# Kernel tuning notes

Measured on AMD Instinct MI355X. Metric: run time of the kernel, lower is better.

Reference implementation:

```python
import jax, jax.numpy as jnp
import numpy as np

BETA = 0.5  # exp-sum normalization exponent (not a true softmax)


def setup_inputs() -> dict:
    key = jax.random.key(0)
    ks = jax.random.split(key, 12)
    b, h = 1024, 200
    item_num, region_num, user_num = 50000, 1000, 10000
    d, hid = 128, 128  # embed_size == hidden_size (required by the bmm reshape)
    std = 0.01
    return {
        "history": jax.random.randint(ks[0], (1, b, h), 0, item_num),
        "target": jax.random.randint(ks[1], (1, b), 0, item_num),
        "history_region": jax.random.randint(ks[2], (1, b, h), 0, region_num),
        "target_region": jax.random.randint(ks[3], (1, b), 0, region_num),
        "history_visit_rate": jax.random.uniform(ks[4], (1, h), dtype=jnp.float32),
        "dist_mat": jax.random.uniform(ks[5], (b, h), dtype=jnp.float32),
        "uid": 7,
        "embed_target": std * jax.random.normal(ks[6], (item_num, d // 2), dtype=jnp.float32),
        "embed_region": std * jax.random.normal(ks[7], (region_num, d // 2), dtype=jnp.float32),
        "embed_dist": std * jax.random.normal(ks[8], (user_num, region_num), dtype=jnp.float32),
        "Wq": jax.random.normal(ks[9], (hid, d), dtype=jnp.float32) * (1.0 / np.sqrt(d)),
        "Wk": jax.random.normal(ks[10], (hid, d), dtype=jnp.float32) * (1.0 / np.sqrt(d)),
        "Wv": jax.random.normal(ks[11], (d, d), dtype=jnp.float32) * (1.0 / np.sqrt(d)),
    }


def reference(history, target, history_region, target_region, history_visit_rate,
              dist_mat, uid, embed_target, embed_region, embed_dist, Wq, Wk, Wv):
    h_idx = history[0]            # [b, h]
    tgt = target[0]               # [b]
    hr = history_region[0]        # [b, h]
    tr = target_region[0]         # [b]
    hv = history_visit_rate[0]    # [h]
    b, hlen = h_idx.shape

    # embedding gathers + concat (target half | region half)
    hist_emb = jnp.concatenate([embed_target[h_idx], embed_region[hr]], axis=-1)  # [b,h,d]
    tgt_emb = jnp.concatenate([embed_target[tgt], embed_region[tr]], axis=-1)     # [b,d]
    hd = embed_dist[uid][hr]      # [b, h]
    td = embed_dist[uid][tr]      # [b]
    d = tgt_emb.shape[1]

    # QKV projections (torch Linear: y = x @ W.T)
    q = tgt_emb @ Wq.T            # [b, d]  (hidden == d)
    k = hist_emb @ Wk.T           # [b, h, d]
    v = hist_emb @ Wv.T           # [b, h, d]

    # faithful to original: key reshaped (NOT transposed) to [b, d, h]
    k_r = k.reshape(b, d, hlen)
    scores = jnp.einsum('bd,bdh->bh', q, k_r) / jnp.sqrt(jnp.float32(d))  # [b,h]

    # exp / beta-normalized attention with equality mask
    mask = (h_idx != tgt[:, None]).astype(scores.dtype)
    exp_A = jnp.exp(scores) * mask                          # [b,h]
    exp_sum = jnp.sum(exp_A, axis=-1) ** BETA               # [b]
    attn = exp_A / exp_sum[:, None]                         # [b,h]

    # geo weights: td @ hd is a vector-matrix product -> [h], broadcast over b
    geo = jnp.exp(-1.0 / (jax.nn.relu(td @ hd) + 1.0) * dist_mat)  # [b,h]

    result1 = v * (attn + geo)[..., None]                   # [b,h,d]
    result2 = hist_emb * jnp.broadcast_to(hv, (b, hlen))[..., None]
    result = result1 + result2                              # [b,h,d]

    pred = jnp.einsum('bhd,bd->b', result, tgt_emb)         # bmm + sum over h
    return jax.nn.sigmoid(pred)
```

## Files before the change

### kernel.cpp

```cpp
#include <hip/hip_runtime.h>

typedef unsigned short USH;
typedef unsigned int   UIN;

static constexpr int Bn = 1024;
static constexpr int Hn = 200;
static constexpr int Dn = 128;
static constexpr int Dh = 64;
static constexpr int NITEM = 50000;
static constexpr int NREG  = 1000;
static constexpr int MT = 64;
static constexpr int AB_A_BLOCKS = (NITEM + MT - 1) / MT;
static constexpr int AB_B_BLOCKS = (NREG  + MT - 1) / MT;
static constexpr int WTS = 132;
static constexpr int ETS = 69;

__device__ __forceinline__ float bf2f(USH u) {
  return __uint_as_float(((UIN)u) << 16);
}
__device__ __forceinline__ float2 pb2f2(UIN p) {
  float2 r;
  r.x = __uint_as_float(p << 16);
  r.y = __uint_as_float(p & 0xffff0000u);
  return r;
}
__device__ __forceinline__ USH f2b(float f) {
  UIN x = __float_as_uint(f);
  return (USH)((x + 0x7fffu + ((x >> 16) & 1u)) >> 16);
}

__global__ __launch_bounds__(256) void g_kernel(
    const int* __restrict__ hregion, const int* __restrict__ tregion,
    const float* __restrict__ embed_dist, const int* __restrict__ uid,
    float* __restrict__ g) {
  int c = threadIdx.x;
  const float* row = embed_dist + (size_t)uid[0] * NREG;
  float acc = 0.f;
  int ibase = blockIdx.x * 16;
  for (int ii = 0; ii < 16; ii++) {
    int i = ibase + ii;
    float td = row[tregion[i]];
    if (c < Hn) acc += td * row[hregion[(size_t)i * Hn + c]];
  }
  if (c < Hn) atomicAdd(&g[c], acc);
}

__global__ __launch_bounds__(256, 2) void ab_kernel(
    const float* __restrict__ Et, const float* __restrict__ Er,
    const float* __restrict__ Wk, USH* __restrict__ A, USH* __restrict__ Bt) {
  __shared__ float wt[64 * WTS];
  __shared__ float et[MT * ETS];
  int blk = blockIdx.x, tid = threadIdx.x;
  const float* E; USH* Out; int nmax, base, koff;
  if (blk < AB_A_BLOCKS) { E = Et; Out = A;  nmax = NITEM; base = blk * MT; koff = 0; }
  else { E = Er; Out = Bt; nmax = NREG; base = (blk - AB_A_BLOCKS) * MT; koff = 64; }

#pragma unroll
  for (int p = 0; p < 8; p++) {
    int idx = p * 256 + tid;
    int row = idx >> 4, c4 = idx & 15;
    float4 w = *reinterpret_cast<const float4*>(Wk + (size_t)row * Dn + koff + c4 * 4);
    wt[(c4 * 4 + 0) * WTS + row] = w.x;
    wt[(c4 * 4 + 1) * WTS + row] = w.y;
    wt[(c4 * 4 + 2) * WTS + row] = w.z;
    wt[(c4 * 4 + 3) * WTS + row] = w.w;
  }
#pragma unroll
  for (int p = 0; p < 4; p++) {
    int idx = p * 256 + tid;
    int m = idx >> 4, c4 = idx & 15;
    int gi = base + m;
    float4 e = make_float4(0.f, 0.f, 0.f, 0.f);
    if (gi < nmax) e = *reinterpret_cast<const float4*>(E + (size_t)gi * Dh + c4 * 4);
    et[m * ETS + c4 * 4 + 0] = e.x;
    et[m * ETS + c4 * 4 + 1] = e.y;
    et[m * ETS + c4 * 4 + 2] = e.z;
    et[m * ETS + c4 * 4 + 3] = e.w;
  }
  __syncthreads();

  int jt = tid & 15, it = tid >> 4;
  const float* wb = wt + jt * 8;
  const float* eb = et + (it * 4) * ETS;
  float c[4][8];
#pragma unroll
  for (int ii = 0; ii < 4; ii++)
#pragma unroll
    for (int jj = 0; jj < 8; jj++) c[ii][jj] = 0.f;

#pragma unroll 2
  for (int k = 0; k < 64; k++) {
    float4 w0 = *reinterpret_cast<const float4*>(wb + (size_t)k * WTS);
    float4 w1 = *reinterpret_cast<const float4*>(wb + (size_t)k * WTS + 4);
    float e0 = eb[k], e1 = eb[ETS + k], e2 = eb[2 * ETS + k], e3 = eb[3 * ETS + k];
    c[0][0] += e0 * w0.x; c[0][1] += e0 * w0.y; c[0][2] += e0 * w0.z; c[0][3] += e0 * w0.w;
    c[0][4] += e0 * w1.x; c[0][5] += e0 * w1.y; c[0][6] += e0 * w1.z; c[0][7] += e0 * w1.w;
    c[1][0] += e1 * w0.x; c[1][1] += e1 * w0.y; c[1][2] += e1 * w0.z; c[1][3] += e1 * w0.w;
    c[1][4] += e1 * w1.x; c[1][5] += e1 * w1.y; c[1][6] += e1 * w1.z; c[1][7] += e1 * w1.w;
    c[2][0] += e2 * w0.x; c[2][1] += e2 * w0.y; c[2][2] += e2 * w0.z; c[2][3] += e2 * w0.w;
    c[2][4] += e2 * w1.x; c[2][5] += e2 * w1.y; c[2][6] += e2 * w1.z; c[2][7] += e2 * w1.w;
    c[3][0] += e3 * w0.x; c[3][1] += e3 * w0.y; c[3][2] += e3 * w0.z; c[3][3] += e3 * w0.w;
    c[3][4] += e3 * w1.x; c[3][5] += e3 * w1.y; c[3][6] += e3 * w1.z; c[3][7] += e3 * w1.w;
  }

#pragma unroll
  for (int ii = 0; ii < 4; ii++) {
    int item = base + it * 4 + ii;
    if (item < nmax) {
      uint4 pk;
      pk.x = (UIN)f2b(c[ii][0]) | ((UIN)f2b(c[ii][1]) << 16);
      pk.y = (UIN)f2b(c[ii][2]) | ((UIN)f2b(c[ii][3]) << 16);
      pk.z = (UIN)f2b(c[ii][4]) | ((UIN)f2b(c[ii][5]) << 16);
      pk.w = (UIN)f2b(c[ii][6]) | ((UIN)f2b(c[ii][7]) << 16);
      *reinterpret_cast<uint4*>(Out + (size_t)item * Dn + jt * 8) = pk;
    }
  }
}

__global__ __launch_bounds__(256, 2) void main_kernel(
    const int* __restrict__ history, const int* __restrict__ target,
    const int* __restrict__ hregion, const int* __restrict__ tregion,
    const float* __restrict__ hv, const float* __restrict__ dist_mat,
    const float* __restrict__ Et, const float* __restrict__ Er,
    const float* __restrict__ Wq, const float* __restrict__ Wv,
    const float* __restrict__ g, const USH* __restrict__ A,
    const USH* __restrict__ Bt, float* __restrict__ out) {
  __shared__ USH kvs[Hn * Dn];
  __shared__ float tgtE[128], qv[128], uv[128];
  __shared__ float qp[256], up[256];
  __shared__ int li[Hn], lr[Hn];
  __shared__ float red[8];
  int i = blockIdx.x, tid = threadIdx.x, lane = tid & 63, wave = tid >> 6;
  int tgt_i = target[i], tr_i = tregion[i];
  const int* hrow = history + (size_t)i * Hn;
  const int* rrow = hregion + (size_t)i * Hn;

  if (tid < Hn) { li[tid] = hrow[tid]; lr[tid] = rrow[tid]; }
  if (tid < 64)       tgtE[tid] = Et[(size_t)tgt_i * Dh + tid];
  else if (tid < 128) tgtE[tid] = Er[(size_t)tr_i * Dh + (tid - 64)];
  __syncthreads();

  {
    int rlane = tid & 31, rgrp = tid >> 5;
#pragma unroll 5
    for (int p = 0; p < 25; p++) {
      int t = p * 8 + rgrp;
      int ia = li[t], ib = lr[t];
      uint2 av = *reinterpret_cast<const uint2*>(A  + (size_t)ia * Dn + rlane * 4);
      uint2 bv = *reinterpret_cast<const uint2*>(Bt + (size_t)ib * Dn + rlane * 4);
      float2 a0 = pb2f2(av.x), a1 = pb2f2(av.y);
      float2 b0 = pb2f2(bv.x), b1 = pb2f2(bv.y);
      uint2 pk;
      pk.x = (UIN)f2b(a0.x + b0.x) | ((UIN)f2b(a0.y + b0.y) << 16);
      pk.y = (UIN)f2b(a1.x + b1.x) | ((UIN)f2b(a1.y + b1.y) << 16);
      *reinterpret_cast<uint2*>(&kvs[t * Dn + rlane * 4]) = pk;
    }
  }

  {
    int jq = tid & 127, hq = tid >> 7;
    const float4* wqp = reinterpret_cast<const float4*>(Wq + (size_t)jq * Dn + hq * 64);
    float qa = 0.f;
#pragma unroll
    for (int k4 = 0; k4 < 16; k4++) {
      float4 w = wqp[k4];
      const float* tv = &tgtE[hq * 64 + k4 * 4];
      qa += w.x * tv[0] + w.y * tv[1] + w.z * tv[2] + w.w * tv[3];
    }
    qp[tid] = qa;
    float ua = 0.f;
#pragma unroll 8
    for (int jj = 0; jj < 64; jj++)
      ua += Wv[(size_t)(hq * 64 + jj) * Dn + jq] * tgtE[hq * 64 + jj];
    up[tid] = ua;
  }
  __syncthreads();
  if (tid < 128) {
    qv[tid] = (qp[tid] + qp[tid + 128]) * 0.088388347648318447f;
    uv[tid] = up[tid] + up[tid + 128];
  }
  __syncthreads();

  float ea = 0.f, sc1 = 0.f, sc2 = 0.f;
  if (tid < Hn) {
    int c = tid;
    float acc = 0.f;
    const USH* kp = &kvs[c];
#pragma unroll 16
    for (int a = 0; a < 128; a++) acc += qv[a] * bf2f(kp[a * 200]);
    int t = tid;
    const float4* ep = reinterpret_cast<const float4*>(Et + (size_t)li[t] * Dh);
    const float4* rp = reinterpret_cast<const float4*>(Er + (size_t)lr[t] * Dh);
    float p1 = 0.f, p2 = 0.f;
#pragma unroll
    for (int k4 = 0; k4 < 16; k4++) {
      float4 e = ep[k4], r = rp[k4];
      const float* u0 = &uv[k4 * 4];        const float* t0 = &tgtE[k4 * 4];
      const float* u1 = &uv[64 + k4 * 4];   const float* t1 = &tgtE[64 + k4 * 4];
      p1 += e.x * u0[0] + e.y * u0[1] + e.z * u0[2] + e.w * u0[3]
          + r.x * u1[0] + r.y * u1[1] + r.z * u1[2] + r.w * u1[3];
      p2 += e.x * t0[0] + e.y * t0[1] + e.z * t0[2] + e.w * t0[3]
          + r.x * t1[0] + r.y * t1[1] + r.z * t1[2] + r.w * t1[3];
    }
    sc1 = p1; sc2 = p2;
    ea = (li[tid] != tgt_i) ? __expf(acc) : 0.f;
  }

  float wsum = ea;
  for (int off = 32; off > 0; off >>= 1) wsum += __shfl_down(wsum, off, 64);
  if (lane == 0) red[wave] = wsum;
  __syncthreads();
  float esum = red[0] + red[1] + red[2] + red[3];
  float inv = esum > 0.f ? 1.f / sqrtf(esum) : 0.f;

  float part = 0.f;
  if (tid < Hn) {
    float attn = ea * inv;
    float gc = g[tid]; gc = gc > 0.f ? gc : 0.f;
    float dm = dist_mat[(size_t)i * Hn + tid];
    float geo = __expf(-dm / (gc + 1.f));
    part = (attn + geo) * sc1 + hv[tid] * sc2;
  }
  __syncthreads();
  for (int off = 32; off > 0; off >>= 1) part += __shfl_down(part, off, 64);
  if (lane == 0) red[wave] = part;
  __syncthreads();
  if (tid == 0) {
    float pred = red[0] + red[1] + red[2] + red[3];
    out[i] = 1.f / (1.f + __expf(-pred));
  }
}

extern "C" void kernel_launch(void* const* d_in, const int* in_sizes, int n_in,
                              void* d_out, int out_size, void* d_ws, size_t ws_size,
                              hipStream_t stream) {
  const int*   history = (const int*)d_in[0];
  const int*   target  = (const int*)d_in[1];
  const int*   hregion = (const int*)d_in[2];
  const int*   tregion = (const int*)d_in[3];
  const float* hv      = (const float*)d_in[4];
  const float* dist    = (const float*)d_in[5];
  const int*   uid     = (const int*)d_in[6];
  const float* Et      = (const float*)d_in[7];
  const float* Er      = (const float*)d_in[8];
  const float* Edist   = (const float*)d_in[9];
  const float* Wq      = (const float*)d_in[10];
  const float* Wk      = (const float*)d_in[11];
  const float* Wv      = (const float*)d_in[12];

  float* g = (float*)d_ws;
  USH* A   = (USH*)((char*)d_ws + 1024);
  USH* Bt  = A + (size_t)NITEM * Dn;
  float* out = (float*)d_out;

  hipMemsetAsync(g, 0, Hn * sizeof(float), stream);
  g_kernel<<<Bn / 16, 256, 0, stream>>>(hregion, tregion, Edist, uid, g);
  ab_kernel<<<AB_A_BLOCKS + AB_B_BLOCKS, 256, 0, stream>>>(Et, Er, Wk, A, Bt);
  main_kernel<<<Bn, 256, 0, stream>>>(history, target, hregion, tregion, hv, dist,
                                      Et, Er, Wq, Wv, g, A, Bt, out);
}
```

Baseline: 180.0 us.

## Emit bf16 raw embeddings, widen K gathers, and simplify projections in main kernel

The projection kernel now also writes bf16 copies of the item and region embedding tables, and the main kernel reads these half-width rows for the value and residual dot products instead of the fp32 tables, gated on workspace size. The K-row gathers use 16-byte loads with 16 lanes per row, and index staging in shared memory plus one barrier are removed. The q and u projections are each done by one half of the block over the full length, and launch bounds allow three blocks per CU. The aim is to cut gather bandwidth and shared memory use, in exchange for extra writes in the projection kernel and bf16 rounding of the embeddings.

Result: faster. 176.1 us (-2.2%).

```diff
diff --git a/kernel.cpp b/kernel.cpp
--- a/kernel.cpp
+++ b/kernel.cpp
@@ -27,6 +27,10 @@
 __device__ __forceinline__ USH f2b(float f) {
   UIN x = __float_as_uint(f);
   return (USH)((x + 0x7fffu + ((x >> 16) & 1u)) >> 16);
+}
+__device__ __forceinline__ UIN addpk(UIN u, UIN v) {
+  float2 a = pb2f2(u), b = pb2f2(v);
+  return (UIN)f2b(a.x + b.x) | ((UIN)f2b(a.y + b.y) << 16);
 }
 
 __global__ __launch_bounds__(256) void g_kernel(
@@ -47,13 +51,14 @@
 
 __global__ __launch_bounds__(256, 2) void ab_kernel(
     const float* __restrict__ Et, const float* __restrict__ Er,
-    const float* __restrict__ Wk, USH* __restrict__ A, USH* __restrict__ Bt) {
+    const float* __restrict__ Wk, USH* __restrict__ A, USH* __restrict__ Bt,
+    USH* __restrict__ Ebr, USH* __restrict__ Err, int emit_raw) {
   __shared__ float wt[64 * WTS];
   __shared__ float et[MT * ETS];
   int blk = blockIdx.x, tid = threadIdx.x;
-  const float* E; USH* Out; int nmax, base, koff;
-  if (blk < AB_A_BLOCKS) { E = Et; Out = A;  nmax = NITEM; base = blk * MT; koff = 0; }
-  else { E = Er; Out = Bt; nmax = NREG; base = (blk - AB_A_BLOCKS) * MT; koff = 64; }
+  const float* E; USH* Out; USH* OutR; int nmax, base, koff;
+  if (blk < AB_A_BLOCKS) { E = Et; Out = A;  OutR = Ebr; nmax = NITEM; base = blk * MT; koff = 0; }
+  else { E = Er; Out = Bt; OutR = Err; nmax = NREG; base = (blk - AB_A_BLOCKS) * MT; koff = 64; }
 
 #pragma unroll
   for (int p = 0; p < 8; p++) {
@@ -78,6 +83,19 @@
     et[m * ETS + c4 * 4 + 3] = e.w;
   }
   __syncthreads();
+
+  if (emit_raw) {
+#pragma unroll
+    for (int q = 0; q < 8; q++) {
+      int idx = q * 256 + tid;
+      int m = idx >> 5, kp = idx & 31;
+      int gi = base + m;
+      if (gi < nmax) {
+        UIN pk = (UIN)f2b(et[m * ETS + 2 * kp]) | ((UIN)f2b(et[m * ETS + 2 * kp + 1]) << 16);
+        *reinterpret_cast<UIN*>(OutR + (size_t)gi * Dh + 2 * kp) = pk;
+      }
+    }
+  }
 
   int jt = tid & 15, it = tid >> 4;
   const float* wb = wt + jt * 8;
@@ -117,67 +135,65 @@
   }
 }
 
-__global__ __launch_bounds__(256, 2) void main_kernel(
+__global__ __launch_bounds__(256, 3) void main_kernel(
     const int* __restrict__ history, const int* __restrict__ target,
     const int* __restrict__ hregion, const int* __restrict__ tregion,
     const float* __restrict__ hv, const float* __restrict__ dist_mat,
     const float* __restrict__ Et, const float* __restrict__ Er,
     const float* __restrict__ Wq, const float* __restrict__ Wv,
     const float* __restrict__ g, const USH* __restrict__ A,
-    const USH* __restrict__ Bt, float* __restrict__ out) {
+    const USH* __restrict__ Bt, const USH* __restrict__ Ebr,
+    const USH* __restrict__ Err, int use_raw, float* __restrict__ out) {
   __shared__ USH kvs[Hn * Dn];
   __shared__ float tgtE[128], qv[128], uv[128];
-  __shared__ float qp[256], up[256];
-  __shared__ int li[Hn], lr[Hn];
   __shared__ float red[8];
   int i = blockIdx.x, tid = threadIdx.x, lane = tid & 63, wave = tid >> 6;
   int tgt_i = target[i], tr_i = tregion[i];
   const int* hrow = history + (size_t)i * Hn;
   const int* rrow = hregion + (size_t)i * Hn;
 
-  if (tid < Hn) { li[tid] = hrow[tid]; lr[tid] = rrow[tid]; }
   if (tid < 64)       tgtE[tid] = Et[(size_t)tgt_i * Dh + tid];
   else if (tid < 128) tgtE[tid] = Er[(size_t)tr_i * Dh + (tid - 64)];
-  __syncthreads();
 
   {
-    int rlane = tid & 31, rgrp = tid >> 5;
-#pragma unroll 5
-    for (int p = 0; p < 25; p++) {
-      int t = p * 8 + rgrp;
-      int ia = li[t], ib = lr[t];
-      uint2 av = *reinterpret_cast<const uint2*>(A  + (size_t)ia * Dn + rlane * 4);
-      uint2 bv = *reinterpret_cast<const uint2*>(Bt + (size_t)ib * Dn + rlane * 4);
-      float2 a0 = pb2f2(av.x), a1 = pb2f2(av.y);
-      float2 b0 = pb2f2(bv.x), b1 = pb2f2(bv.y);
-      uint2 pk;
-      pk.x = (UIN)f2b(a0.x + b0.x) | ((UIN)f2b(a0.y + b0.y) << 16);
-      pk.y = (UIN)f2b(a1.x + b1.x) | ((UIN)f2b(a1.y + b1.y) << 16);
-      *reinterpret_cast<uint2*>(&kvs[t * Dn + rlane * 4]) = pk;
-    }
-  }
-
-  {
-    int jq = tid & 127, hq = tid >> 7;
-    const float4* wqp = reinterpret_cast<const float4*>(Wq + (size_t)jq * Dn + hq * 64);
-    float qa = 0.f;
-#pragma unroll
-    for (int k4 = 0; k4 < 16; k4++) {
-      float4 w = wqp[k4];
-      const float* tv = &tgtE[hq * 64 + k4 * 4];
-      qa += w.x * tv[0] + w.y * tv[1] + w.z * tv[2] + w.w * tv[3];
-    }
-    qp[tid] = qa;
-    float ua = 0.f;
+    int rlane = tid & 15, rgrp = tid >> 4;
+#pragma unroll
+    for (int p = 0; p < 13; p++) {
+      int t = p * 16 + rgrp;
+      if (t < Hn) {
+        int ia = hrow[t], ib = rrow[t];
+        uint4 av = *reinterpret_cast<const uint4*>(A  + (size_t)ia * Dn + rlane * 8);
+        uint4 bv = *reinterpret_cast<const uint4*>(Bt + (size_t)ib * Dn + rlane * 8);
+        uint4 pk;
+        pk.x = addpk(av.x, bv.x); pk.y = addpk(av.y, bv.y);
+        pk.z = addpk(av.z, bv.z); pk.w = addpk(av.w, bv.w);
+        *reinterpret_cast<uint4*>(&kvs[t * Dn + rlane * 8]) = pk;
+      }
+    }
+  }
+  __syncthreads();
+
+  if (tid < 128) {
+    int j = tid; float acc = 0.f;
+    const float4* wp = reinterpret_cast<const float4*>(Wq + (size_t)j * Dn);
+#pragma unroll
+    for (int q4 = 0; q4 < 32; q4++) {
+      float4 w = wp[q4];
+      const float* tv = &tgtE[q4 * 4];
+      acc += w.x * tv[0] + w.y * tv[1] + w.z * tv[2] + w.w * tv[3];
+    }
+    qv[j] = acc * 0.088388347648318447f;
+  } else {
+    int d = tid - 128;
+    float a0 = 0.f, a1 = 0.f, a2 = 0.f, a3 = 0.f;
 #pragma unroll 8
-    for (int jj = 0; jj < 64; jj++)
-      ua += Wv[(size_t)(hq * 64 + jj) * Dn + jq] * tgtE[hq * 64 + jj];
-    up[tid] = ua;
-  }
-  __syncthreads();
-  if (tid < 128) {
-    qv[tid] = (qp[tid] + qp[tid + 128]) * 0.088388347648318447f;
-    uv[tid] = up[tid] + up[tid + 128];
+    for (int j = 0; j < 128; j += 4) {
+      a0 += Wv[(size_t)(j + 0) * Dn + d] * tgtE[j + 0];
+      a1 += Wv[(size_t)(j + 1) * Dn + d] * tgtE[j + 1];
+      a2 += Wv[(size_t)(j + 2) * Dn + d] * tgtE[j + 2];
+      a3 += Wv[(size_t)(j + 3) * Dn + d] * tgtE[j + 3];
+    }
+    uv[d] = (a0 + a1) + (a2 + a3);
   }
   __syncthreads();
 
@@ -188,22 +204,43 @@
     const USH* kp = &kvs[c];
 #pragma unroll 16
     for (int a = 0; a < 128; a++) acc += qv[a] * bf2f(kp[a * 200]);
-    int t = tid;
-    const float4* ep = reinterpret_cast<const float4*>(Et + (size_t)li[t] * Dh);
-    const float4* rp = reinterpret_cast<const float4*>(Er + (size_t)lr[t] * Dh);
+    int ia2 = hrow[tid], ib2 = rrow[tid];
     float p1 = 0.f, p2 = 0.f;
-#pragma unroll
-    for (int k4 = 0; k4 < 16; k4++) {
-      float4 e = ep[k4], r = rp[k4];
-      const float* u0 = &uv[k4 * 4];        const float* t0 = &tgtE[k4 * 4];
-      const float* u1 = &uv[64 + k4 * 4];   const float* t1 = &tgtE[64 + k4 * 4];
-      p1 += e.x * u0[0] + e.y * u0[1] + e.z * u0[2] + e.w * u0[3]
-          + r.x * u1[0] + r.y * u1[1] + r.z * u1[2] + r.w * u1[3];
-      p2 += e.x * t0[0] + e.y * t0[1] + e.z * t0[2] + e.w * t0[3]
-          + r.x * t1[0] + r.y * t1[1] + r.z * t1[2] + r.w * t1[3];
+    if (use_raw) {
+      const uint4* epu = reinterpret_cast<const uint4*>(Ebr + (size_t)ia2 * Dh);
+      const uint4* rpu = reinterpret_cast<const uint4*>(Err + (size_t)ib2 * Dh);
+#pragma unroll
+      for (int k8 = 0; k8 < 8; k8++) {
+        uint4 e = epu[k8], r = rpu[k8];
+        float2 e0 = pb2f2(e.x), e1 = pb2f2(e.y), e2 = pb2f2(e.z), e3 = pb2f2(e.w);
+        float2 r0 = pb2f2(r.x), r1 = pb2f2(r.y), r2 = pb2f2(r.z), r3 = pb2f2(r.w);
+        const float* u0 = &uv[k8 * 8];       const float* t0 = &tgtE[k8 * 8];
+        const float* u1 = &uv[64 + k8 * 8];  const float* t1 = &tgtE[64 + k8 * 8];
+        p1 += e0.x * u0[0] + e0.y * u0[1] + e1.x * u0[2] + e1.y * u0[3]
+            + e2.x * u0[4] + e2.y * u0[5] + e3.x * u0[6] + e3.y * u0[7]
+            + r0.x * u1[0] + r0.y * u1[1] + r1.x * u1[2] + r1.y * u1[3]
+            + r2.x * u1[4] + r2.y * u1[5] + r3.x * u1[6] + r3.y * u1[7];
+        p2 += e0.x * t0[0] + e0.y * t0[1] + e1.x * t0[2] + e1.y * t0[3]
+            + e2.x * t0[4] + e2.y * t0[5] + e3.x * t0[6] + e3.y * t0[7]
+            + r0.x * t1[0] + r0.y * t1[1] + r1.x * t1[2] + r1.y * t1[3]
+            + r2.x * t1[4] + r2.y * t1[5] + r3.x * t1[6] + r3.y * t1[7];
+      }
+    } else {
+      const float4* ep = reinterpret_cast<const float4*>(Et + (size_t)ia2 * Dh);
+      const float4* rp = reinterpret_cast<const float4*>(Er + (size_t)ib2 * Dh);
+#pragma unroll
+      for (int k4 = 0; k4 < 16; k4++) {
+        float4 e = ep[k4], r = rp[k4];
+        const float* u0 = &uv[k4 * 4];        const float* t0 = &tgtE[k4 * 4];
+        const float* u1 = &uv[64 + k4 * 4];   const float* t1 = &tgtE[64 + k4 * 4];
+        p1 += e.x * u0[0] + e.y * u0[1] + e.z * u0[2] + e.w * u0[3]
+            + r.x * u1[0] + r.y * u1[1] + r.z * u1[2] + r.w * u1[3];
+        p2 += e.x * t0[0] + e.y * t0[1] + e.z * t0[2] + e.w * t0[3]
+            + r.x * t1[0] + r.y * t1[1] + r.z * t1[2] + r.w * t1[3];
+      }
     }
     sc1 = p1; sc2 = p2;
-    ea = (li[tid] != tgt_i) ? __expf(acc) : 0.f;
+    ea = (ia2 != tgt_i) ? __expf(acc) : 0.f;
   }
 
   float wsum = ea;
@@ -251,11 +288,18 @@
   float* g = (float*)d_ws;
   USH* A   = (USH*)((char*)d_ws + 1024);
   USH* Bt  = A + (size_t)NITEM * Dn;
+  USH* Ebr = Bt + (size_t)NREG * Dn;
+  USH* Err = Ebr + (size_t)NITEM * Dh;
+  size_t need_raw = 1024 + 2 * ((size_t)NITEM * Dn + (size_t)NREG * Dn +
+                                (size_t)NITEM * Dh + (size_t)NREG * Dh);
+  int use_raw = (ws_size >= need_raw) ? 1 : 0;
   float* out = (float*)d_out;
 
   hipMemsetAsync(g, 0, Hn * sizeof(float), stream);
   g_kernel<<<Bn / 16, 256, 0, stream>>>(hregion, tregion, Edist, uid, g);
-  ab_kernel<<<AB_A_BLOCKS + AB_B_BLOCKS, 256, 0, stream>>>(Et, Er, Wk, A, Bt);
+  ab_kernel<<<AB_A_BLOCKS + AB_B_BLOCKS, 256, 0, stream>>>(Et, Er, Wk, A, Bt,
+                                                           Ebr, Err, use_raw);
   main_kernel<<<Bn, 256, 0, stream>>>(history, target, hregion, tregion, hv, dist,
-                                      Et, Er, Wq, Wv, g, A, Bt, out);
-}
+                                      Et, Er, Wq, Wv, g, A, Bt, Ebr, Err, use_raw,
+                                      out);
+}
```
